# Optimization experiments

Measured on AMD Instinct MI355X. Metric: run time of the kernel, lower is better.

The kernel has to match this reference:

```python
import jax, jax.numpy as jnp
import numpy as np

B, T, HID = 1, 256, 2048
H, D = 16, 128
KD = H * D
CONV = 4
MAX_CG = 30
LAMB_LB = 0.25
NORM_EPS = 1e-5


def setup_inputs() -> dict:
    key = jax.random.key(0)
    ks = jax.random.split(key, 10)
    s = 0.02
    init_lamb = float(np.log(np.exp(1.0 - LAMB_LB) - 1.0))  # softplus^-1(1 - lower_bound)
    return {
        "hidden_states": jax.random.normal(ks[0], (B, T, HID), jnp.float32),
        "Wq": jax.random.normal(ks[1], (HID, KD), jnp.float32) * s,
        "Wk": jax.random.normal(ks[2], (HID, KD), jnp.float32) * s,
        "Wv": jax.random.normal(ks[3], (HID, KD), jnp.float32) * s,
        "Wa": jax.random.normal(ks[4], (HID, H), jnp.float32) * s,
        "ba": jnp.full((H,), 2.0, jnp.float32),
        "Wb": jax.random.normal(ks[5], (HID, H), jnp.float32) * s,
        "bb": jnp.zeros((H,), jnp.float32),
        "conv_wq": jax.random.normal(ks[6], (KD, CONV), jnp.float32) * s,
        "conv_wk": jax.random.normal(ks[7], (KD, CONV), jnp.float32) * s,
        "lambda_params": jnp.full((KD,), init_lamb, jnp.float32),
        "o_norm_w": jnp.ones((D,), jnp.float32),
        "Wo": jax.random.normal(ks[8], (KD, HID), jnp.float32) * s,
    }


def short_conv_silu(x, w):
    # depthwise causal conv over time; x [b,t,c], w [c,k]
    k = w.shape[1]
    xp = jnp.pad(x, ((0, 0), (k - 1, 0), (0, 0)))
    t = x.shape[1]
    y = xp[:, 0:t, :] * w[:, 0]
    for i in range(1, k):
        y = y + xp[:, i:i + t, :] * w[:, i]
    return jax.nn.silu(y)


def l2norm(x):
    return x * jax.lax.rsqrt(jnp.sum(x * x, -1, keepdims=True) + 1e-6)


def rmsnorm(x, w):
    return x * jax.lax.rsqrt(jnp.mean(x * x, -1, keepdims=True) + NORM_EPS) * w


def cg_solve(A, b):
    # solve A x = b per (batch, head) with fixed CG iterations, x0 = 0
    matvec = lambda p: jnp.einsum('bhij,bhj->bhi', A, p)
    x0 = jnp.zeros_like(b)
    rs0 = jnp.sum(b * b, -1)

    def body(i, st):
        xc, r, p, rs = st
        Ap = matvec(p)
        alpha = rs / (jnp.sum(p * Ap, -1) + 1e-12)
        xc = xc + alpha[..., None] * p
        r = r - alpha[..., None] * Ap
        rs_n = jnp.sum(r * r, -1)
        p = r + (rs_n / (rs + 1e-12))[..., None] * p
        return xc, r, p, rs_n

    xf, _, _, _ = jax.lax.fori_loop(0, MAX_CG, body, (x0, b, b, rs0))
    return xf


def mesa_recurrence(q, k, v, g, beta, lamb_diag):
    # q,k,v [b,t,h,d]; g,beta [b,t,h]; lamb_diag [h,d,d]
    def step(carry, inp):
        h_kk, h_kv = carry
        qt, kt, vt, gt, bt = inp
        decay = jnp.exp(gt)[..., None, None]
        b_ = bt[..., None, None]
        h_kk = h_kk * decay + b_ * (kt[..., :, None] * kt[..., None, :])
        h_kv = h_kv * decay + b_ * (kt[..., :, None] * vt[..., None, :])
        A = h_kk + lamb_diag[None]
        q_star = cg_solve(A, qt)
        ot = jnp.einsum('bhk,bhkv->bhv', q_star, h_kv)
        return (h_kk, h_kv), ot

    init = (jnp.zeros((B, H, D, D), q.dtype), jnp.zeros((B, H, D, D), q.dtype))
    xs = (q.transpose(1, 0, 2, 3), k.transpose(1, 0, 2, 3), v.transpose(1, 0, 2, 3),
          g.transpose(1, 0, 2), beta.transpose(1, 0, 2))
    _, o = jax.lax.scan(step, init, xs)
    return o.transpose(1, 0, 2, 3)  # [b,t,h,d]


def reference(hidden_states, Wq, Wk, Wv, Wa, ba, Wb, bb, conv_wq, conv_wk,
              lambda_params, o_norm_w, Wo):
    x = hidden_states
    q = short_conv_silu(x @ Wq, conv_wq)
    k = short_conv_silu(x @ Wk, conv_wk)
    v = x @ Wv
    q = l2norm(q.reshape(B, T, H, D))
    k = l2norm(k.reshape(B, T, H, D))
    v = v.reshape(B, T, H, D)
    beta = jax.nn.sigmoid(x @ Wb + bb)          # [b,t,h]
    g = jax.nn.log_sigmoid(x @ Wa + ba)          # [b,t,h]
    lamb = (jax.nn.softplus(lambda_params) + LAMB_LB).reshape(H, D)
    lamb_diag = lamb[:, :, None] * jnp.eye(D, dtype=lamb.dtype)  # [h,d,d]
    o = mesa_recurrence(q, k, v, g, beta, lamb_diag)
    o = rmsnorm(o, o_norm_w)
    o = o.reshape(B, T, KD) @ Wo
    return o
```

## Files before the change

### kernel.cpp

```cpp
#include <hip/hip_runtime.h>
#include <math.h>

#define TT 256
#define HIDDEN 2048
#define NH 16
#define HD 128
#define KDIM 2048
#define NCG 30

typedef _Float16 h2 __attribute__((ext_vector_type(2)));
typedef _Float16 h4 __attribute__((ext_vector_type(4)));
typedef _Float16 half8 __attribute__((ext_vector_type(8)));
typedef float floatx4 __attribute__((ext_vector_type(4)));

__device__ __forceinline__ float wave_sum64(float v) {
#pragma unroll
    for (int off = 32; off > 0; off >>= 1) v += __shfl_xor(v, off, 64);
    return v;
}

__device__ __forceinline__ half8 cvt8(const float4 x, const float4 y) {
    half8 f;
    f[0] = (_Float16)x.x; f[1] = (_Float16)x.y; f[2] = (_Float16)x.z; f[3] = (_Float16)x.w;
    f[4] = (_Float16)y.x; f[5] = (_Float16)y.y; f[6] = (_Float16)y.z; f[7] = (_Float16)y.w;
    return f;
}

__device__ __forceinline__ void glds16(const void* g, void* l) {
    __builtin_amdgcn_global_load_lds(
        (const __attribute__((address_space(1))) void*)g,
        (__attribute__((address_space(3))) void*)l, 16, 0, 0);
}

__global__ __launch_bounds__(256) void wtrans_kernel(
    const float* __restrict__ W0, const float* __restrict__ W1,
    const float* __restrict__ W2, const float* __restrict__ W3,
    _Float16* __restrict__ T0, _Float16* __restrict__ T1,
    _Float16* __restrict__ T2, _Float16* __restrict__ T3)
{
    __shared__ float tile[64][68];
    const int z = blockIdx.z;
    const float* __restrict__ W = (z == 0) ? W0 : (z == 1) ? W1 : (z == 2) ? W2 : W3;
    _Float16* __restrict__ T = (z == 0) ? T0 : (z == 1) ? T1 : (z == 2) ? T2 : T3;
    const int k0 = blockIdx.x * 64, n0 = blockIdx.y * 64;
    const int tid = threadIdx.x;
#pragma unroll
    for (int p = 0; p < 4; p++) {
        const int idx = p * 256 + tid;
        const int r = idx >> 4, c = (idx & 15) * 4;
        const float4 v = *(const float4*)&W[(size_t)(k0 + r) * KDIM + n0 + c];
        tile[r][c] = v.x; tile[r][c + 1] = v.y; tile[r][c + 2] = v.z; tile[r][c + 3] = v.w;
    }
    __syncthreads();
#pragma unroll
    for (int p = 0; p < 2; p++) {
        const int c = p * 256 + tid;
        const int dn = c >> 3, c8 = c & 7;
        const int gk = k0 + c8 * 8, gn = n0 + dn;
        const int nt = gn >> 7, nn = gn & 127;
        const int kt = gk >> 5, kc = (gk >> 3) & 3;
        half8 o;
#pragma unroll
        for (int j = 0; j < 8; j++) o[j] = (_Float16)tile[c8 * 8 + j][dn];
        *(half8*)&T[(size_t)(((nt * 64 + kt) * 4 + kc)) * 1024 + nn * 8] = o;
    }
}

__global__ __launch_bounds__(256) void wab_trans_kernel(
    const float* __restrict__ Wa, const float* __restrict__ Wb, float* __restrict__ Tab)
{
    const int b = blockIdx.x;
    const int h = threadIdx.x & 15, kl = threadIdx.x >> 4;
    for (int p = 0; p < 16; p++) {
        const int k = b * 256 + p * 16 + kl;
        Tab[h * KDIM + k] = Wa[k * NH + h];
        Tab[(16 + h) * KDIM + k] = Wb[k * NH + h];
    }
}

#define ASTR 72
__global__ __launch_bounds__(256) void gemm_kernel(
    const float* __restrict__ A,
    const _Float16* __restrict__ Bb0, const _Float16* __restrict__ Bb1,
    const _Float16* __restrict__ Bb2,
    float* __restrict__ C0, float* __restrict__ C1, float* __restrict__ C2,
    int nTilesPerMat)
{
    __shared__ __align__(16) _Float16 Bsh[2][8192];
    __shared__ __align__(16) _Float16 Ash[2][32 * ASTR];

    const int tid = threadIdx.x, lane = tid & 63, w = tid >> 6;
    const int q = lane >> 4, l16 = lane & 15;
    const int nt = blockIdx.x, mt = blockIdx.y;
    const int mat = nt / nTilesPerMat;
    const int ntile = nt - mat * nTilesPerMat;
    const int n0 = ntile * 128;
    const _Float16* __restrict__ Bb = (mat == 0) ? Bb0 : (mat == 1) ? Bb1 : Bb2;
    float* __restrict__ C = (mat == 0) ? C0 : (mat == 1) ? C1 : C2;
    const int m0 = mt * 32;

    const _Float16* __restrict__ Btile = Bb + (size_t)ntile * 262144;
    const int ar = tid >> 3, ac = (tid & 7) * 8;
    const float* __restrict__ Ap = &A[(size_t)(m0 + ar) * KDIM + ac];

    floatx4 acc[2][2] = {};
    float4 ax, ay;

#pragma unroll
    for (int i = 0; i < 4; i++)
        glds16(Btile + (size_t)((w * 4 + i) * 64 + lane) * 8, &Bsh[0][(w * 4 + i) * 512]);
    ax = *(const float4*)&Ap[0]; ay = *(const float4*)&Ap[4];
    *(half8*)&Ash[0][ar * ASTR + ac] = cvt8(ax, ay);
    ax = *(const float4*)&Ap[64]; ay = *(const float4*)&Ap[68];
    __syncthreads();

    const int NSTEP = KDIM / 64;
    for (int s = 0; s < NSTEP; s++) {
        const int cur = s & 1;
        if (s + 1 < NSTEP) {
            const _Float16* src = Btile + (size_t)(s + 1) * 8192;
#pragma unroll
            for (int i = 0; i < 4; i++)
                glds16(src + (size_t)((w * 4 + i) * 64 + lane) * 8, &Bsh[cur ^ 1][(w * 4 + i) * 512]);
        }
#pragma unroll
        for (int kk = 0; kk < 2; kk++) {
            const half8 bf0 = *(const half8*)&Bsh[cur][kk * 4096 + q * 1024 + (w * 32 + l16) * 8];
            const half8 bf1 = *(const half8*)&Bsh[cur][kk * 4096 + q * 1024 + (w * 32 + 16 + l16) * 8];
            const half8 af0 = *(const half8*)&Ash[cur][l16 * ASTR + kk * 32 + q * 8];
            const half8 af1 = *(const half8*)&Ash[cur][(16 + l16) * ASTR + kk * 32 + q * 8];
            acc[0][0] = __builtin_amdgcn_mfma_f32_16x16x32_f16(af0, bf0, acc[0][0], 0, 0, 0);
            acc[0][1] = __builtin_amdgcn_mfma_f32_16x16x32_f16(af0, bf1, acc[0][1], 0, 0, 0);
            acc[1][0] = __builtin_amdgcn_mfma_f32_16x16x32_f16(af1, bf0, acc[1][0], 0, 0, 0);
            acc[1][1] = __builtin_amdgcn_mfma_f32_16x16x32_f16(af1, bf1, acc[1][1], 0, 0, 0);
        }
        if (s + 1 < NSTEP) {
            *(half8*)&Ash[cur ^ 1][ar * ASTR + ac] = cvt8(ax, ay);
            if (s + 2 < NSTEP) {
                ax = *(const float4*)&Ap[(s + 2) * 64];
                ay = *(const float4*)&Ap[(s + 2) * 64 + 4];
            }
        }
        __syncthreads();
    }

#pragma unroll
    for (int r = 0; r < 4; r++) {
        C[(size_t)(m0 + q * 4 + r) * KDIM + n0 + w * 32 + l16] = acc[0][0][r];
        C[(size_t)(m0 + q * 4 + r) * KDIM + n0 + w * 32 + 16 + l16] = acc[0][1][r];
        C[(size_t)(m0 + 16 + q * 4 + r) * KDIM + n0 + w * 32 + l16] = acc[1][0][r];
        C[(size_t)(m0 + 16 + q * 4 + r) * KDIM + n0 + w * 32 + 16 + l16] = acc[1][1][r];
    }
}

__global__ __launch_bounds__(256) void ab_kernel(
    const float* __restrict__ X, const float* __restrict__ Tab,
    const float* __restrict__ ba, const float* __restrict__ bb,
    float* __restrict__ g, float* __restrict__ beta)
{
    const int t = blockIdx.x;
    const int lane = threadIdx.x & 63, w = threadIdx.x >> 6;
    for (int oi = 0; oi < 8; oi++) {
        const int o = w * 8 + oi;
        const int h = o & 15, which = o >> 4;
        float acc = 0.f;
#pragma unroll
        for (int i = 0; i < 8; i++) {
            const int kk = lane * 4 + i * 256;
            const float4 xv = *(const float4*)&X[t * HIDDEN + kk];
            const float4 wv = *(const float4*)&Tab[o * KDIM + kk];
            acc = fmaf(xv.x, wv.x, acc); acc = fmaf(xv.y, wv.y, acc);
            acc = fmaf(xv.z, wv.z, acc); acc = fmaf(xv.w, wv.w, acc);
        }
        acc = wave_sum64(acc);
        if (lane == 0) {
            if (which == 0) {
                const float z = acc + ba[h];
                g[t * NH + h] = fminf(z, 0.f) - log1pf(__expf(-fabsf(z)));
            } else {
                const float z = acc + bb[h];
                beta[t * NH + h] = 1.f / (1.f + __expf(-z));
            }
        }
    }
}

__global__ __launch_bounds__(256) void prep_kernel(const float* __restrict__ g,
                                                   float* __restrict__ G,
                                                   const float* __restrict__ lp,
                                                   float* __restrict__ lamb)
{
    __shared__ float gs[TT * NH];
    const int tid = threadIdx.x;
    for (int i = tid; i < KDIM; i += 256) {
        const float x = lp[i];
        lamb[i] = fmaxf(x, 0.f) + log1pf(__expf(-fabsf(x))) + 0.25f;
    }
    for (int i = tid; i < TT * NH; i += 256) gs[i] = g[i];
    __syncthreads();
    if (tid < NH) {
        float run = 0.f;
        for (int t = 0; t < TT; t++) { run += gs[t * NH + tid]; gs[t * NH + tid] = run; }
    }
    __syncthreads();
    for (int i = tid; i < TT * NH; i += 256) G[i] = gs[i];
}

__global__ __launch_bounds__(256) void conv_silu_l2_kernel(
    const float* __restrict__ q_pre, const float* __restrict__ k_pre,
    const float* __restrict__ cwq, const float* __restrict__ cwk,
    float* __restrict__ qn, float* __restrict__ kn)
{
    const int t = blockIdx.x, h = blockIdx.y;
    const int which = threadIdx.x >> 7, d = threadIdx.x & 127;
    const int w = threadIdx.x >> 6;
    const int c = h * HD + d;
    const float* pre = which ? k_pre : q_pre;
    const float* cw  = which ? cwk : cwq;
    float y = 0.f;
#pragma unroll
    for (int i = 0; i < 4; i++) {
        const int ts = t - 3 + i;
        if (ts >= 0) y = fmaf(pre[ts * KDIM + c], cw[c * 4 + i], y);
    }
    const float s = y / (1.f + __expf(-y));
    float v = s * s;
#pragma unroll
    for (int off = 32; off > 0; off >>= 1) v += __shfl_down(v, off, 64);
    __shared__ float red[4];
    if ((threadIdx.x & 63) == 0) red[w] = v;
    __syncthreads();
    const float sum = red[which * 2] + red[which * 2 + 1];
    float* dst = which ? kn : qn;
    dst[t * KDIM + c] = s * rsqrtf(sum + 1e-6f);
}

#define KTSTR 264
#define PSTR 136
#define YSTR 264
#define MESA_LDS (128 * KTSTR * 2 + 16 * PSTR * 2 + 16 * YSTR * 2 + 64 * 4)

template<int SMAX>
__device__ __forceinline__ void mesa_cg(
    const float* __restrict__ qn, const float* __restrict__ kn, const float* __restrict__ vv,
    const float* __restrict__ G, const float* __restrict__ bet, const float* __restrict__ lamb,
    const float* __restrict__ onw, float* __restrict__ out,
    int h, int t0, _Float16* Kt, _Float16* Psh, _Float16* Ysh, float* red)
{
    constexpr int NSUB1 = SMAX / 64;
    constexpr int NK2   = SMAX / 32;

    const int tid = threadIdx.x, lane = tid & 63, w = tid >> 6;
    const int quad = lane >> 4, l16 = lane & 15;
    const int tmy = t0 + l16;
    const int dbase = w * 32;

    {
        const int sd = tid & 127, sg = tid >> 7;
        for (int s0 = 0; s0 < SMAX; s0 += 8) {
            const int sb = s0 + sg * 4;
            h4 kv;
#pragma unroll
            for (int j = 0; j < 4; j++) kv[j] = (_Float16)kn[((sb + j) * NH + h) * HD + sd];
            *(h4*)&Kt[sd * KTSTR + sb] = kv;
        }
    }

    half8 K1[NSUB1][4];
#pragma unroll
    for (int ii = 0; ii < NSUB1; ii++) {
        const int srow = 16 * (w + 4 * ii) + l16;
        const float* kp = &kn[(srow * NH + h) * HD];
#pragma unroll
        for (int kk = 0; kk < 4; kk++) {
            const float4 a = *(const float4*)&kp[kk * 32 + quad * 8];
            const float4 b = *(const float4*)&kp[kk * 32 + quad * 8 + 4];
            K1[ii][kk] = cvt8(a, b);
        }
    }
    const float Gt = G[tmy * NH + h];
    float Wm[NSUB1][4];
#pragma unroll
    for (int ii = 0; ii < NSUB1; ii++)
#pragma unroll
        for (int r = 0; r < 4; r++) {
            const int s = 16 * (w + 4 * ii) + quad * 4 + r;
            Wm[ii][r] = (s <= tmy) ? bet[s * NH + h] * __expf(Gt - G[s * NH + h]) : 0.f;
        }
    float lam[8], xv[8], rv[8], pv[8];
#pragma unroll
    for (int ss = 0; ss < 2; ss++)
#pragma unroll
        for (int r = 0; r < 4; r++) {
            const int e = ss * 4 + r;
            const int d = dbase + ss * 16 + quad * 4 + r;
            lam[e] = lamb[h * HD + d];
            const float b = qn[(tmy * NH + h) * HD + d];
            xv[e] = 0.f; rv[e] = b; pv[e] = b;
        }
    float rs = 0.f;
#pragma unroll
    for (int e = 0; e < 8; e++) rs += rv[e] * rv[e];
    rs += __shfl_xor(rs, 16, 64); rs += __shfl_xor(rs, 32, 64);

    auto writeP = [&](const float* src) {
#pragma unroll
        for (int ss = 0; ss < 2; ss++) {
            h4 ph;
            ph.x = (_Float16)src[ss * 4 + 0]; ph.y = (_Float16)src[ss * 4 + 1];
            ph.z = (_Float16)src[ss * 4 + 2]; ph.w = (_Float16)src[ss * 4 + 3];
            *(h4*)&Psh[l16 * PSTR + dbase + ss * 16 + quad * 4] = ph;
        }
    };
    writeP(pv);

    for (int it = 0; it <= NCG; it++) {
        __syncthreads();
        floatx4 acc1[NSUB1] = {};
#pragma unroll
        for (int kk = 0; kk < 4; kk++) {
            const half8 bf = *(const half8*)&Psh[l16 * PSTR + kk * 32 + quad * 8];
#pragma unroll
            for (int ii = 0; ii < NSUB1; ii++)
                acc1[ii] = __builtin_amdgcn_mfma_f32_16x16x32_f16(K1[ii][kk], bf, acc1[ii], 0, 0, 0);
        }
#pragma unroll
        for (int ii = 0; ii < NSUB1; ii++) {
            h4 yh;
            yh.x = (_Float16)(Wm[ii][0] * acc1[ii][0]);
            yh.y = (_Float16)(Wm[ii][1] * acc1[ii][1]);
            yh.z = (_Float16)(Wm[ii][2] * acc1[ii][2]);
            yh.w = (_Float16)(Wm[ii][3] * acc1[ii][3]);
            *(h4*)&Ysh[l16 * YSTR + 16 * (w + 4 * ii) + quad * 4] = yh;
        }
        __syncthreads();
        if (it == NCG) break;

        floatx4 acc2[2] = {};
#pragma unroll
        for (int kk = 0; kk < NK2; kk++) {
            const half8 bf = *(const half8*)&Ysh[l16 * YSTR + kk * 32 + quad * 8];
#pragma unroll
            for (int ss = 0; ss < 2; ss++) {
                const half8 af = *(const half8*)&Kt[(dbase + ss * 16 + l16) * KTSTR + kk * 32 + quad * 8];
                acc2[ss] = __builtin_amdgcn_mfma_f32_16x16x32_f16(af, bf, acc2[ss], 0, 0, 0);
            }
        }
        float Ap[8], pAp = 0.f;
#pragma unroll
        for (int ss = 0; ss < 2; ss++)
#pragma unroll
            for (int r = 0; r < 4; r++) {
                const int e = ss * 4 + r;
                Ap[e] = acc2[ss][r] + lam[e] * pv[e];
                pAp += pv[e] * Ap[e];
            }
        pAp += __shfl_xor(pAp, 16, 64); pAp += __shfl_xor(pAp, 32, 64);
        const float alpha = rs / (pAp + 1e-12f);
        float rsn = 0.f;
#pragma unroll
        for (int e = 0; e < 8; e++) {
            xv[e] = fmaf(alpha, pv[e], xv[e]);
            rv[e] = fmaf(-alpha, Ap[e], rv[e]);
            rsn += rv[e] * rv[e];
        }
        rsn += __shfl_xor(rsn, 16, 64); rsn += __shfl_xor(rsn, 32, 64);
        const float bcg = rsn / (rs + 1e-12f);
#pragma unroll
        for (int e = 0; e < 8; e++) pv[e] = fmaf(bcg, pv[e], rv[e]);
        rs = rsn;
        writeP(it == NCG - 1 ? xv : pv);
    }

    floatx4 accO[2] = {};
#pragma unroll
    for (int kk = 0; kk < NK2; kk++) {
        const half8 af = *(const half8*)&Ysh[l16 * YSTR + kk * 32 + quad * 8];
#pragma unroll
        for (int ss = 0; ss < 2; ss++) {
            half8 bf;
#pragma unroll
            for (int jj = 0; jj < 8; jj++) {
                const int s = kk * 32 + quad * 8 + jj;
                bf[jj] = (_Float16)vv[(s * NH + h) * HD + dbase + ss * 16 + l16];
            }
            accO[ss] = __builtin_amdgcn_mfma_f32_16x16x32_f16(af, bf, accO[ss], 0, 0, 0);
        }
    }

    float part[4];
#pragma unroll
    for (int r = 0; r < 4; r++) {
        part[r] = accO[0][r] * accO[0][r] + accO[1][r] * accO[1][r];
#pragma unroll
        for (int off = 1; off < 16; off <<= 1) part[r] += __shfl_xor(part[r], off, 64);
    }
    if (l16 == 0) {
#pragma unroll
        for (int r = 0; r < 4; r++) red[w * 16 + quad * 4 + r] = part[r];
    }
    __syncthreads();
    const float w0 = onw[dbase + l16], w1 = onw[dbase + 16 + l16];
#pragma unroll
    for (int r = 0; r < 4; r++) {
        const int qr = quad * 4 + r;
        const float sumd = red[qr] + red[16 + qr] + red[32 + qr] + red[48 + qr];
        const float sc = rsqrtf(sumd * (1.f / HD) + 1e-5f);
        const int trow = ((t0 + qr) * NH + h) * HD;
        out[trow + dbase + l16] = accO[0][r] * sc * w0;
        out[trow + dbase + 16 + l16] = accO[1][r] * sc * w1;
    }
}

__global__ __launch_bounds__(256) void mesa_kernel(
    const float* __restrict__ qn, const float* __restrict__ kn, const float* __restrict__ vv,
    const float* __restrict__ G, const float* __restrict__ bet, const float* __restrict__ lamb,
    const float* __restrict__ onw, float* __restrict__ out)
{
    extern __shared__ char smem_raw[];
    _Float16* Kt  = (_Float16*)smem_raw;
    _Float16* Psh = (_Float16*)(smem_raw + 128 * KTSTR * 2);
    _Float16* Ysh = (_Float16*)(smem_raw + 128 * KTSTR * 2 + 16 * PSTR * 2);
    float* red = (float*)(smem_raw + 128 * KTSTR * 2 + 16 * PSTR * 2 + 16 * YSTR * 2);
    const int h = blockIdx.x, jb = blockIdx.y, t0 = jb * 16;
    switch (jb >> 2) {
        case 0:  mesa_cg<64> (qn, kn, vv, G, bet, lamb, onw, out, h, t0, Kt, Psh, Ysh, red); break;
        case 1:  mesa_cg<128>(qn, kn, vv, G, bet, lamb, onw, out, h, t0, Kt, Psh, Ysh, red); break;
        case 2:  mesa_cg<192>(qn, kn, vv, G, bet, lamb, onw, out, h, t0, Kt, Psh, Ysh, red); break;
        default: mesa_cg<256>(qn, kn, vv, G, bet, lamb, onw, out, h, t0, Kt, Psh, Ysh, red); break;
    }
}

extern "C" void kernel_launch(void* const* d_in, const int* in_sizes, int n_in,
                              void* d_out, int out_size, void* d_ws, size_t ws_size,
                              hipStream_t stream)
{
    (void)in_sizes; (void)n_in; (void)out_size; (void)ws_size;
    const float* x   = (const float*)d_in[0];
    const float* Wq  = (const float*)d_in[1];
    const float* Wk  = (const float*)d_in[2];
    const float* Wv  = (const float*)d_in[3];
    const float* Wa  = (const float*)d_in[4];
    const float* ba  = (const float*)d_in[5];
    const float* Wb  = (const float*)d_in[6];
    const float* bb  = (const float*)d_in[7];
    const float* cwq = (const float*)d_in[8];
    const float* cwk = (const float*)d_in[9];
    const float* lp  = (const float*)d_in[10];
    const float* onw = (const float*)d_in[11];
    const float* Wo  = (const float*)d_in[12];

    char* wsb = (char*)d_ws;
    float* q_pre = (float*)wsb;
    float* k_pre = q_pre + 524288;
    float* v     = k_pre + 524288;
    float* qn    = v + 524288;
    float* kn    = qn + 524288;
    float* g     = kn + 524288;
    float* beta  = g + 4096;
    float* G     = beta + 4096;
    float* lamb  = G + 4096;
    size_t off = ((size_t)((char*)(lamb + 2048) - wsb) + 1023) & ~(size_t)1023;
    _Float16* WtQ = (_Float16*)(wsb + off);
    _Float16* WtK = WtQ + (size_t)KDIM * KDIM;
    _Float16* WtV = WtK + (size_t)KDIM * KDIM;
    _Float16* WtO = WtV + (size_t)KDIM * KDIM;
    float* Tab    = (float*)(WtO + (size_t)KDIM * KDIM);
    float* onorm  = q_pre;
    float* outp   = (float*)d_out;

    wtrans_kernel<<<dim3(32, 32, 4), 256, 0, stream>>>(Wq, Wk, Wv, Wo, WtQ, WtK, WtV, WtO);
    wab_trans_kernel<<<8, 256, 0, stream>>>(Wa, Wb, Tab);

    gemm_kernel<<<dim3(48, 8), 256, 0, stream>>>(x, WtQ, WtK, WtV, q_pre, k_pre, v, 16);
    ab_kernel<<<dim3(TT), 256, 0, stream>>>(x, Tab, ba, bb, g, beta);
    prep_kernel<<<1, 256, 0, stream>>>(g, G, lp, lamb);
    conv_silu_l2_kernel<<<dim3(TT, NH), 256, 0, stream>>>(q_pre, k_pre, cwq, cwk, qn, kn);

    (void)hipFuncSetAttribute((const void*)mesa_kernel,
                              hipFuncAttributeMaxDynamicSharedMemorySize, MESA_LDS);
    mesa_kernel<<<dim3(NH, 16), 256, MESA_LDS, stream>>>(qn, kn, v, G, beta, lamb, onw, onorm);

    gemm_kernel<<<dim3(16, 8), 256, 0, stream>>>(onorm, WtO, WtO, WtO, outp, outp, outp, 16);
}
```

Before: 255.7 us.

## Keep K-transpose and V fragments in registers, split MFMA accumulators in CG loop

The transposed K tile used in the CG matvec moves from LDS into per-thread register fragments, and the V fragments for the output product are loaded once before the loop instead of gathered afterwards. MFMA accumulation chains are split into two independent accumulators to hide MFMA latency, and the launch bound declares one block per SM. This removes LDS traffic and the LDS staging pass on every CG iteration, but greatly raises register pressure (up to 8 K fragments plus 16 V fragments at SMAX=256), which risks spilling.

```diff
diff --git a/kernel.cpp b/kernel.cpp
--- a/kernel.cpp
+++ b/kernel.cpp
@@ -235,17 +235,15 @@
     dst[t * KDIM + c] = s * rsqrtf(sum + 1e-6f);
 }
 
-#define KTSTR 264
 #define PSTR 136
 #define YSTR 264
-#define MESA_LDS (128 * KTSTR * 2 + 16 * PSTR * 2 + 16 * YSTR * 2 + 64 * 4)
 
 template<int SMAX>
 __device__ __forceinline__ void mesa_cg(
     const float* __restrict__ qn, const float* __restrict__ kn, const float* __restrict__ vv,
     const float* __restrict__ G, const float* __restrict__ bet, const float* __restrict__ lamb,
     const float* __restrict__ onw, float* __restrict__ out,
-    int h, int t0, _Float16* Kt, _Float16* Psh, _Float16* Ysh, float* red)
+    int h, int t0, _Float16* Psh, _Float16* Ysh, float* red)
 {
     constexpr int NSUB1 = SMAX / 64;
     constexpr int NK2   = SMAX / 32;
@@ -255,17 +253,6 @@
     const int tmy = t0 + l16;
     const int dbase = w * 32;
 
-    {
-        const int sd = tid & 127, sg = tid >> 7;
-        for (int s0 = 0; s0 < SMAX; s0 += 8) {
-            const int sb = s0 + sg * 4;
-            h4 kv;
-#pragma unroll
-            for (int j = 0; j < 4; j++) kv[j] = (_Float16)kn[((sb + j) * NH + h) * HD + sd];
-            *(h4*)&Kt[sd * KTSTR + sb] = kv;
-        }
-    }
-
     half8 K1[NSUB1][4];
 #pragma unroll
     for (int ii = 0; ii < NSUB1; ii++) {
@@ -278,6 +265,35 @@
             K1[ii][kk] = cvt8(a, b);
         }
     }
+
+    half8 KtF[2][NK2];
+#pragma unroll
+    for (int ss = 0; ss < 2; ss++) {
+        const int d = dbase + ss * 16 + l16;
+#pragma unroll
+        for (int kk = 0; kk < NK2; kk++) {
+#pragma unroll
+            for (int j = 0; j < 8; j++) {
+                const int s = kk * 32 + quad * 8 + j;
+                KtF[ss][kk][j] = (_Float16)kn[(s * NH + h) * HD + d];
+            }
+        }
+    }
+
+    half8 Vf[NK2][2];
+#pragma unroll
+    for (int kk = 0; kk < NK2; kk++) {
+#pragma unroll
+        for (int ss = 0; ss < 2; ss++) {
+            const int dv = dbase + ss * 16 + l16;
+#pragma unroll
+            for (int j = 0; j < 8; j++) {
+                const int s = kk * 32 + quad * 8 + j;
+                Vf[kk][ss][j] = (_Float16)vv[(s * NH + h) * HD + dv];
+            }
+        }
+    }
+
     const float Gt = G[tmy * NH + h];
     float Wm[NSUB1][4];
 #pragma unroll
@@ -316,34 +332,38 @@
 
     for (int it = 0; it <= NCG; it++) {
         __syncthreads();
-        floatx4 acc1[NSUB1] = {};
-#pragma unroll
-        for (int kk = 0; kk < 4; kk++) {
-            const half8 bf = *(const half8*)&Psh[l16 * PSTR + kk * 32 + quad * 8];
-#pragma unroll
-            for (int ii = 0; ii < NSUB1; ii++)
-                acc1[ii] = __builtin_amdgcn_mfma_f32_16x16x32_f16(K1[ii][kk], bf, acc1[ii], 0, 0, 0);
+        floatx4 acc1a[NSUB1] = {}, acc1b[NSUB1] = {};
+#pragma unroll
+        for (int kk = 0; kk < 2; kk++) {
+            const half8 bfa = *(const half8*)&Psh[l16 * PSTR + kk * 32 + quad * 8];
+            const half8 bfb = *(const half8*)&Psh[l16 * PSTR + (kk + 2) * 32 + quad * 8];
+#pragma unroll
+            for (int ii = 0; ii < NSUB1; ii++) {
+                acc1a[ii] = __builtin_amdgcn_mfma_f32_16x16x32_f16(K1[ii][kk], bfa, acc1a[ii], 0, 0, 0);
+                acc1b[ii] = __builtin_amdgcn_mfma_f32_16x16x32_f16(K1[ii][kk + 2], bfb, acc1b[ii], 0, 0, 0);
+            }
         }
 #pragma unroll
         for (int ii = 0; ii < NSUB1; ii++) {
             h4 yh;
-            yh.x = (_Float16)(Wm[ii][0] * acc1[ii][0]);
-            yh.y = (_Float16)(Wm[ii][1] * acc1[ii][1]);
-            yh.z = (_Float16)(Wm[ii][2] * acc1[ii][2]);
-            yh.w = (_Float16)(Wm[ii][3] * acc1[ii][3]);
+            yh.x = (_Float16)(Wm[ii][0] * (acc1a[ii][0] + acc1b[ii][0]));
+            yh.y = (_Float16)(Wm[ii][1] * (acc1a[ii][1] + acc1b[ii][1]));
+            yh.z = (_Float16)(Wm[ii][2] * (acc1a[ii][2] + acc1b[ii][2]));
+            yh.w = (_Float16)(Wm[ii][3] * (acc1a[ii][3] + acc1b[ii][3]));
             *(h4*)&Ysh[l16 * YSTR + 16 * (w + 4 * ii) + quad * 4] = yh;
         }
         __syncthreads();
         if (it == NCG) break;
 
-        floatx4 acc2[2] = {};
-#pragma unroll
-        for (int kk = 0; kk < NK2; kk++) {
-            const half8 bf = *(const half8*)&Ysh[l16 * YSTR + kk * 32 + quad * 8];
+        floatx4 acc2a[2] = {}, acc2b[2] = {};
+#pragma unroll
+        for (int kk = 0; kk < NK2; kk += 2) {
+            const half8 bf0 = *(const half8*)&Ysh[l16 * YSTR + kk * 32 + quad * 8];
+            const half8 bf1 = *(const half8*)&Ysh[l16 * YSTR + (kk + 1) * 32 + quad * 8];
 #pragma unroll
             for (int ss = 0; ss < 2; ss++) {
-                const half8 af = *(const half8*)&Kt[(dbase + ss * 16 + l16) * KTSTR + kk * 32 + quad * 8];
-                acc2[ss] = __builtin_amdgcn_mfma_f32_16x16x32_f16(af, bf, acc2[ss], 0, 0, 0);
+                acc2a[ss] = __builtin_amdgcn_mfma_f32_16x16x32_f16(KtF[ss][kk], bf0, acc2a[ss], 0, 0, 0);
+                acc2b[ss] = __builtin_amdgcn_mfma_f32_16x16x32_f16(KtF[ss][kk + 1], bf1, acc2b[ss], 0, 0, 0);
             }
         }
         float Ap[8], pAp = 0.f;
@@ -352,8 +372,8 @@
 #pragma unroll
             for (int r = 0; r < 4; r++) {
                 const int e = ss * 4 + r;
-                Ap[e] = acc2[ss][r] + lam[e] * pv[e];
-                pAp += pv[e] * Ap[e];
+                Ap[e] = (acc2a[ss][r] + acc2b[ss][r]) + lam[e] * pv[e];
+                pAp = fmaf(pv[e], Ap[e], pAp);
             }
         pAp += __shfl_xor(pAp, 16, 64); pAp += __shfl_xor(pAp, 32, 64);
         const float alpha = rs / (pAp + 1e-12f);
@@ -362,7 +382,7 @@
         for (int e = 0; e < 8; e++) {
             xv[e] = fmaf(alpha, pv[e], xv[e]);
             rv[e] = fmaf(-alpha, Ap[e], rv[e]);
-            rsn += rv[e] * rv[e];
+            rsn = fmaf(rv[e], rv[e], rsn);
         }
         rsn += __shfl_xor(rsn, 16, 64); rsn += __shfl_xor(rsn, 32, 64);
         const float bcg = rsn / (rs + 1e-12f);
@@ -372,21 +392,22 @@
         writeP(it == NCG - 1 ? xv : pv);
     }
 
-    floatx4 accO[2] = {};
-#pragma unroll
-    for (int kk = 0; kk < NK2; kk++) {
-        const half8 af = *(const half8*)&Ysh[l16 * YSTR + kk * 32 + quad * 8];
+    floatx4 accOa[2] = {}, accOb[2] = {};
+#pragma unroll
+    for (int kk = 0; kk < NK2; kk += 2) {
+        const half8 af0 = *(const half8*)&Ysh[l16 * YSTR + kk * 32 + quad * 8];
+        const half8 af1 = *(const half8*)&Ysh[l16 * YSTR + (kk + 1) * 32 + quad * 8];
 #pragma unroll
         for (int ss = 0; ss < 2; ss++) {
-            half8 bf;
-#pragma unroll
-            for (int jj = 0; jj < 8; jj++) {
-                const int s = kk * 32 + quad * 8 + jj;
-                bf[jj] = (_Float16)vv[(s * NH + h) * HD + dbase + ss * 16 + l16];
-            }
-            accO[ss] = __builtin_amdgcn_mfma_f32_16x16x32_f16(af, bf, accO[ss], 0, 0, 0);
-        }
-    }
+            accOa[ss] = __builtin_amdgcn_mfma_f32_16x16x32_f16(af0, Vf[kk][ss], accOa[ss], 0, 0, 0);
+            accOb[ss] = __builtin_amdgcn_mfma_f32_16x16x32_f16(af1, Vf[kk + 1][ss], accOb[ss], 0, 0, 0);
+        }
+    }
+    float accO[2][4];
+#pragma unroll
+    for (int ss = 0; ss < 2; ss++)
+#pragma unroll
+        for (int r = 0; r < 4; r++) accO[ss][r] = accOa[ss][r] + accOb[ss][r];
 
     float part[4];
 #pragma unroll
@@ -412,22 +433,20 @@
     }
 }
 
-__global__ __launch_bounds__(256) void mesa_kernel(
+__global__ __launch_bounds__(256, 1) void mesa_kernel(
     const float* __restrict__ qn, const float* __restrict__ kn, const float* __restrict__ vv,
     const float* __restrict__ G, const float* __restrict__ bet, const float* __restrict__ lamb,
     const float* __restrict__ onw, float* __restrict__ out)
 {
-    extern __shared__ char smem_raw[];
-    _Float16* Kt  = (_Float16*)smem_raw;
-    _Float16* Psh = (_Float16*)(smem_raw + 128 * KTSTR * 2);
-    _Float16* Ysh = (_Float16*)(smem_raw + 128 * KTSTR * 2 + 16 * PSTR * 2);
-    float* red = (float*)(smem_raw + 128 * KTSTR * 2 + 16 * PSTR * 2 + 16 * YSTR * 2);
+    __shared__ __align__(16) _Float16 Psh[16 * PSTR];
+    __shared__ __align__(16) _Float16 Ysh[16 * YSTR];
+    __shared__ float red[64];
     const int h = blockIdx.x, jb = blockIdx.y, t0 = jb * 16;
     switch (jb >> 2) {
-        case 0:  mesa_cg<64> (qn, kn, vv, G, bet, lamb, onw, out, h, t0, Kt, Psh, Ysh, red); break;
-        case 1:  mesa_cg<128>(qn, kn, vv, G, bet, lamb, onw, out, h, t0, Kt, Psh, Ysh, red); break;
-        case 2:  mesa_cg<192>(qn, kn, vv, G, bet, lamb, onw, out, h, t0, Kt, Psh, Ysh, red); break;
-        default: mesa_cg<256>(qn, kn, vv, G, bet, lamb, onw, out, h, t0, Kt, Psh, Ysh, red); break;
+        case 0:  mesa_cg<64> (qn, kn, vv, G, bet, lamb, onw, out, h, t0, Psh, Ysh, red); break;
+        case 1:  mesa_cg<128>(qn, kn, vv, G, bet, lamb, onw, out, h, t0, Psh, Ysh, red); break;
+        case 2:  mesa_cg<192>(qn, kn, vv, G, bet, lamb, onw, out, h, t0, Psh, Ysh, red); break;
+        default: mesa_cg<256>(qn, kn, vv, G, bet, lamb, onw, out, h, t0, Psh, Ysh, red); break;
     }
 }
 
@@ -477,9 +496,7 @@
     prep_kernel<<<1, 256, 0, stream>>>(g, G, lp, lamb);
     conv_silu_l2_kernel<<<dim3(TT, NH), 256, 0, stream>>>(q_pre, k_pre, cwq, cwk, qn, kn);
 
-    (void)hipFuncSetAttribute((const void*)mesa_kernel,
-                              hipFuncAttributeMaxDynamicSharedMemorySize, MESA_LDS);
-    mesa_kernel<<<dim3(NH, 16), 256, MESA_LDS, stream>>>(qn, kn, v, G, beta, lamb, onw, onorm);
+    mesa_kernel<<<dim3(NH, 16), 256, 0, stream>>>(qn, kn, v, G, beta, lamb, onw, onorm);
 
     gemm_kernel<<<dim3(16, 8), 256, 0, stream>>>(onorm, WtO, WtO, WtO, outp, outp, outp, 16);
 }
```

Result: no change. 254.8 us (-0.4%).
